# Performance work log

Measured on AMD Instinct MI355X. Metric: run time of the kernel, lower is better.

The kernel has to match this reference:

```python
import jax, jax.numpy as jnp
import numpy as np
from jax import lax

USER_NUM = 100000
COMP_NUM = 50000
ENTITY_NUM = USER_NUM + COMP_NUM + 2  # 150002
N_ACTIVE = USER_NUM + COMP_NUM        # 150000 valid graph nodes
REL_NUM = 200
D = 128
T = 12        # timesteps
E = 250000    # edges per timestep
S = 20000     # seed (LSTM-updated) nodes per timestep
B = 1024      # user batch
USER_ID_MAX = 99999


def setup_inputs() -> dict:
    key = jax.random.key(0)
    ks = jax.random.split(key, 16)
    ent_emb = jax.random.normal(ks[0], (ENTITY_NUM, D), jnp.float32) * 0.02
    c0_emb = jax.random.normal(ks[1], (ENTITY_NUM, D), jnp.float32) * 0.02
    rel_emb = jax.random.normal(ks[2], (REL_NUM, D), jnp.float32) * 0.02
    W_ih = jax.random.normal(ks[3], (4 * D, D), jnp.float32) * (1.0 / np.sqrt(D))
    W_hh = jax.random.normal(ks[4], (4 * D, D), jnp.float32) * (1.0 / np.sqrt(D))
    b_ih = jax.random.normal(ks[5], (4 * D,), jnp.float32) * 0.01
    b_hh = jax.random.normal(ks[6], (4 * D,), jnp.float32) * 0.01
    src = jax.random.randint(ks[7], (T, E), 0, N_ACTIVE, jnp.int32)
    dst = jax.random.randint(ks[8], (T, E), 0, N_ACTIVE, jnp.int32)
    rel_idx = jax.random.randint(ks[9], (T, E), 0, REL_NUM, jnp.int32)
    # unique seed nodes per timestep (scatter targets must not collide)
    seed_keys = jax.random.split(ks[10], T)
    seed_idx = jax.vmap(lambda k: jax.random.permutation(k, N_ACTIVE)[:S])(seed_keys).astype(jnp.int32)
    user_batch = jax.random.randint(ks[11], (B,), 0, USER_NUM, jnp.int32)
    comp_target = jax.random.randint(ks[12], (B,), 0, COMP_NUM, jnp.int32)
    job_target = jax.random.randint(ks[13], (B,), 0, REL_NUM // 2, jnp.int32)
    return {"ent_emb": ent_emb, "c0_emb": c0_emb, "rel_emb": rel_emb,
            "W_ih": W_ih, "W_hh": W_hh, "b_ih": b_ih, "b_hh": b_hh,
            "src": src, "dst": dst, "rel_idx": rel_idx, "seed_idx": seed_idx,
            "user_batch": user_batch, "comp_target": comp_target, "job_target": job_target}


def reference(ent_emb, c0_emb, rel_emb, W_ih, W_hh, b_ih, b_hh,
              src, dst, rel_idx, seed_idx, user_batch, comp_target, job_target):
    def step(carry, xs):
        h, c = carry                       # [N, D] node_emb / cx
        s, d, r, seed = xs
        # msg_GCN: m = src_node_emb * rel_emb[rel]; reduce_GCN: mean over mailbox
        m = h[s] * rel_emb[r]              # [E, D]
        msum = jax.ops.segment_sum(m, d, num_segments=ENTITY_NUM)
        cnt = jax.ops.segment_sum(jnp.ones((E,), h.dtype), d, num_segments=ENTITY_NUM)
        x = h + msum / jnp.maximum(cnt, 1.0)[:, None]   # update_node: node_emb + node_emb2
        # LSTMCell on seed nodes only (input = aggregated emb, state = pre-agg emb, cx)
        xi, hp, cp = x[seed], h[seed], c[seed]          # [S, D]
        gates = xi @ W_ih.T + b_ih + hp @ W_hh.T + b_hh  # [S, 4D]
        ig, fg, gg, og = jnp.split(gates, 4, axis=-1)
        cn = jax.nn.sigmoid(fg) * cp + jax.nn.sigmoid(ig) * jnp.tanh(gg)
        hn = jax.nn.sigmoid(og) * jnp.tanh(cn)
        return (x.at[seed].set(hn), c.at[seed].set(cn)), None

    (h, _c), _ = lax.scan(step, (ent_emb, c0_emb), (src, dst, rel_idx, seed_idx))

    u = h[user_batch]                                   # [B, D] user time embeddings
    # company softmax-CE (logsumexp over all companies)
    tc = ent_emb[comp_target + USER_ID_MAX + 1]
    all_c = ent_emb[USER_ID_MAX + 1: USER_ID_MAX + 1 + COMP_NUM]  # [COMP_NUM, D]
    pos_c = jnp.sum(u * tc, axis=1)
    comp_loss = -jnp.sum(pos_c - jax.nn.logsumexp(u @ all_c.T, axis=1))
    # job (relation) softmax-CE over rel_num // 2 jobs
    tj = rel_emb[job_target]
    all_j = rel_emb[: REL_NUM // 2]
    pos_j = jnp.sum(u * tj, axis=1)
    job_loss = -jnp.sum(pos_j - jax.nn.logsumexp(u @ all_j.T, axis=1))
    return jnp.stack([comp_loss, job_loss])
```

## Files before the change

kernel.cpp:

```cpp
#include <hip/hip_runtime.h>
#include <math.h>

typedef __attribute__((ext_vector_type(8))) short short8;
typedef __attribute__((ext_vector_type(8))) unsigned short u16x8;
typedef __attribute__((ext_vector_type(4))) float f32x4;

#define USER_NUM_  100000
#define COMP_NUM_  50000
#define EN         150002
#define REL_NUM_   200
#define DD         128
#define TT         12
#define EE         250000
#define SS         20000
#define BB         1024
#define NBLK       587
#define PPART      125
#define TILES_PP   25
#define NB         37
#define BSH        12
#define CHUNK      4096
#define NCH        62

__device__ inline unsigned short f2bf(float f) {
    unsigned u = __float_as_uint(f);
    unsigned r = (u + 0x7fffu + ((u >> 16) & 1u)) >> 16;
    return (unsigned short)r;
}

__device__ inline float bf2f(unsigned short u) {
    return __uint_as_float((unsigned)u << 16);
}

__device__ inline float sigmoidf_(float x) { return 1.f / (1.f + __expf(-x)); }

__device__ inline void lse_push(float v, float& m, float& s) {
    if (v <= m) { s += __expf(v - m); }
    else { s = s * __expf(m - v) + 1.f; m = v; }
}

__device__ inline void lse_merge(float& M, float& S, float M2, float S2) {
    float Mn = fmaxf(M, M2);
    S = S * __expf(M - Mn) + S2 * __expf(M2 - Mn);
    M = Mn;
}

__global__ __launch_bounds__(256) void packBF_k(const float* __restrict__ src, ushort4* __restrict__ dst, int n4) {
    int i = blockIdx.x * 256 + threadIdx.x;
    if (i >= n4) return;
    float4 v = ((const float4*)src)[i];
    ushort4 o;
    o.x = f2bf(v.x); o.y = f2bf(v.y); o.z = f2bf(v.z); o.w = f2bf(v.w);
    dst[i] = o;
}

__global__ __launch_bounds__(256) void zero_i32_k(int* __restrict__ p, int n) {
    int i = blockIdx.x * 256 + threadIdx.x;
    if (i < n) p[i] = 0;
}

__global__ __launch_bounds__(256) void prepW_k(const float* __restrict__ Wih, const float* __restrict__ Whh,
                                               const float* __restrict__ bih, const float* __restrict__ bhh,
                                               short* __restrict__ Wt, float* __restrict__ bsum) {
    int n = blockIdx.x;
    int k = threadIdx.x;
    float v = (k < 128) ? Wih[n * 128 + k] : Whh[n * 128 + (k - 128)];
    Wt[n * 256 + k] = (short)f2bf(v);
    if (k == 0) bsum[n] = bih[n] + bhh[n];
}

__global__ __launch_bounds__(256) void binA_k(const int* __restrict__ dst, int* __restrict__ bcnt,
                                              int t0) {
    int slot = blockIdx.y;
    int tid = threadIdx.x;
    int c0 = blockIdx.x * CHUNK;
    int w = tid >> 6;
    __shared__ int lcnt[4][NB];
    for (int i = tid; i < 4 * NB; i += 256) ((int*)lcnt)[i] = 0;
    __syncthreads();
#pragma unroll
    for (int i = 0; i < 16; ++i) {
        int e = c0 + i * 256 + tid;
        if (e < EE) {
            int d = __builtin_nontemporal_load(&dst[(size_t)(t0 + slot) * EE + e]);
            atomicAdd(&lcnt[w][d >> BSH], 1);
        }
    }
    __syncthreads();
    if (tid < NB)
        atomicAdd(&bcnt[slot * NB + tid], lcnt[0][tid] + lcnt[1][tid] + lcnt[2][tid] + lcnt[3][tid]);
}

__global__ __launch_bounds__(64) void binScan_k(const int* __restrict__ bcnt, int* __restrict__ bbase,
                                                int* __restrict__ bcur, int nt) {
    int slot = threadIdx.x;
    if (slot >= nt) return;
    int b = 0;
    for (int c = 0; c < NB; ++c) {
        bbase[slot * (NB + 1) + c] = b;
        bcur[slot * NB + c] = b;
        b += bcnt[slot * NB + c];
    }
    bbase[slot * (NB + 1) + NB] = b;
}

__global__ __launch_bounds__(256) void binB_k(const int* __restrict__ src, const int* __restrict__ dst,
                                              const int* __restrict__ rel, int* __restrict__ bcur,
                                              int2* __restrict__ bucketed, int t0) {
    int slot = blockIdx.y;
    int tid = threadIdx.x;
    int c0 = blockIdx.x * CHUNK;
    __shared__ int lcnt[NB], lbase[NB], gbase[NB], lcur[NB];
    __shared__ int2 stage[CHUNK];
    if (tid < NB) lcnt[tid] = 0;
    __syncthreads();

    int myb[16]; int2 myv[16];
#pragma unroll
    for (int i = 0; i < 16; ++i) {
        int e = c0 + i * 256 + tid;
        if (e < EE) {
            size_t gi = (size_t)(t0 + slot) * EE + e;
            int d = __builtin_nontemporal_load(&dst[gi]);
            int s = __builtin_nontemporal_load(&src[gi]);
            int r = __builtin_nontemporal_load(&rel[gi]);
            myb[i] = d >> BSH;
            myv[i] = make_int2(d, s | (r << 18));
            atomicAdd(&lcnt[myb[i]], 1);
        } else myb[i] = -1;
    }
    __syncthreads();
    if (tid == 0) {
        int b = 0;
        for (int c = 0; c < NB; ++c) { lbase[c] = b; b += lcnt[c]; }
    }
    __syncthreads();
    if (tid < NB) {
        gbase[tid] = (lcnt[tid] > 0) ? atomicAdd(&bcur[slot * NB + tid], lcnt[tid]) : 0;
        lcur[tid] = lbase[tid];
    }
    __syncthreads();
#pragma unroll
    for (int i = 0; i < 16; ++i) {
        if (myb[i] >= 0) {
            int p = atomicAdd(&lcur[myb[i]], 1);
            stage[p] = myv[i];
        }
    }
    __syncthreads();
    int w = tid >> 6, lane = tid & 63;
    int2* bout = bucketed + (size_t)slot * EE;
    for (int b = w; b < NB; b += 4) {
        int cnt = lcnt[b], lb = lbase[b], gb = gbase[b];
        for (int j = lane; j < cnt; j += 64)
            bout[gb + j] = stage[lb + j];
    }
}

__global__ __launch_bounds__(256) void histB_k(const int2* __restrict__ bucketed,
                                               const int* __restrict__ bbase,
                                               int* __restrict__ startp) {
    int b = blockIdx.x, slot = blockIdx.y;
    int tid = threadIdx.x;
    int base_ent = b << BSH;
    int nloc = EN - base_ent; if (nloc > 4096) nloc = 4096;
    __shared__ int lcnt[4096];
    for (int i = tid; i < nloc; i += 256) lcnt[i] = 0;
    __syncthreads();
    int e0 = bbase[slot * (NB + 1) + b], e1 = bbase[slot * (NB + 1) + b + 1];
    for (int e = e0 + tid; e < e1; e += 256) {
        int2 ed = bucketed[(size_t)slot * EE + e];
        atomicAdd(&lcnt[ed.x - base_ent], 1);
    }
    __syncthreads();
    for (int i = tid; i < nloc; i += 256) startp[(size_t)slot * EN + base_ent + i] = lcnt[i];
}

__global__ __launch_bounds__(256) void scanA_k(int* __restrict__ startp, int* __restrict__ bsums) {
    int slot = blockIdx.y;
    int tid = threadIdx.x;
    int i = blockIdx.x * 256 + tid;
    int v = (i < EN) ? startp[slot * EN + i] : 0;
    __shared__ int lds[256];
    lds[tid] = v; __syncthreads();
#pragma unroll
    for (int o = 1; o < 256; o <<= 1) {
        int x = (tid >= o) ? lds[tid - o] : 0;
        __syncthreads();
        lds[tid] += x;
        __syncthreads();
    }
    if (i < EN) startp[slot * EN + i] = lds[tid] - v;
    if (tid == 255) bsums[slot * NBLK + blockIdx.x] = lds[tid];
}

__global__ __launch_bounds__(1024) void scanB_k(int* __restrict__ bsums) {
    int slot = blockIdx.x;
    int tid = threadIdx.x;
    int v = (tid < NBLK) ? bsums[slot * NBLK + tid] : 0;
    __shared__ int lds[1024];
    lds[tid] = v; __syncthreads();
#pragma unroll
    for (int o = 1; o < 1024; o <<= 1) {
        int x = (tid >= o) ? lds[tid - o] : 0;
        __syncthreads();
        lds[tid] += x;
        __syncthreads();
    }
    if (tid < NBLK) bsums[slot * NBLK + tid] = lds[tid] - v;
}

__global__ __launch_bounds__(256) void scanC_k(int* __restrict__ startp, const int* __restrict__ bsums) {
    int slot = blockIdx.y;
    int i = blockIdx.x * 256 + threadIdx.x;
    if (i < EN) startp[slot * EN + i] += bsums[slot * NBLK + blockIdx.x];
}

__global__ __launch_bounds__(256) void scatB_k(const int2* __restrict__ bucketed,
                                               const int* __restrict__ bbase,
                                               int* __restrict__ startp, int* __restrict__ pairs) {
    int b = blockIdx.x, slot = blockIdx.y;
    int tid = threadIdx.x;
    int base_ent = b << BSH;
    int nloc = EN - base_ent; if (nloc > 4096) nloc = 4096;
    __shared__ int lcur[4096];
    for (int i = tid; i < nloc; i += 256) lcur[i] = startp[(size_t)slot * EN + base_ent + i];
    __syncthreads();
    int e0 = bbase[slot * (NB + 1) + b], e1 = bbase[slot * (NB + 1) + b + 1];
    for (int e = e0 + tid; e < e1; e += 256) {
        int2 ed = bucketed[(size_t)slot * EE + e];
        int pos = atomicAdd(&lcur[ed.x - base_ent], 1);
        pairs[(size_t)slot * EE + pos] = ed.y;
    }
    __syncthreads();
    for (int i = tid; i < nloc; i += 256) startp[(size_t)slot * EN + base_ent + i] = lcur[i];
}

__global__ __launch_bounds__(256) void agg_k(const unsigned short* __restrict__ hold,
                                             unsigned short* __restrict__ hnew,
                                             const unsigned short* __restrict__ Rbf,
                                             const int* __restrict__ endp_all,
                                             const int* __restrict__ pairs, int slot) {
    int tid = threadIdx.x;
    int d = blockIdx.x * 16 + (tid >> 4);
    int l = tid & 15;
    if (d >= EN) return;
    const int* endp = endp_all + (size_t)slot * EN;
    int e0 = (d > 0) ? endp[d - 1] : 0;
    int e1 = endp[d];
    const int* pp = pairs + (size_t)slot * EE;
    float acc[8];
#pragma unroll
    for (int j = 0; j < 8; ++j) acc[j] = 0.f;
    int e = e0;
    for (; e + 2 <= e1; e += 2) {
        int pk0 = pp[e], pk1 = pp[e + 1];
        u16x8 h0 = *(const u16x8*)(hold + (size_t)(pk0 & 0x3FFFF) * DD + l * 8);
        u16x8 r0 = *(const u16x8*)(Rbf + (size_t)(pk0 >> 18) * DD + l * 8);
        u16x8 h1 = *(const u16x8*)(hold + (size_t)(pk1 & 0x3FFFF) * DD + l * 8);
        u16x8 r1 = *(const u16x8*)(Rbf + (size_t)(pk1 >> 18) * DD + l * 8);
#pragma unroll
        for (int j = 0; j < 8; ++j)
            acc[j] = fmaf(bf2f(h1[j]), bf2f(r1[j]), fmaf(bf2f(h0[j]), bf2f(r0[j]), acc[j]));
    }
    if (e < e1) {
        int pk0 = pp[e];
        u16x8 h0 = *(const u16x8*)(hold + (size_t)(pk0 & 0x3FFFF) * DD + l * 8);
        u16x8 r0 = *(const u16x8*)(Rbf + (size_t)(pk0 >> 18) * DD + l * 8);
#pragma unroll
        for (int j = 0; j < 8; ++j)
            acc[j] = fmaf(bf2f(h0[j]), bf2f(r0[j]), acc[j]);
    }
    u16x8 hd = *(const u16x8*)(hold + (size_t)d * DD + l * 8);
    int c = e1 - e0;
    float inv = (c > 0) ? 1.f / (float)c : 0.f;
    u16x8 o;
#pragma unroll
    for (int j = 0; j < 8; ++j) o[j] = f2bf(fmaf(acc[j], inv, bf2f(hd[j])));
    *(u16x8*)(hnew + (size_t)d * DD + l * 8) = o;
}

__global__ __launch_bounds__(256) void lstm_k(const unsigned short* __restrict__ hold,
                                              unsigned short* __restrict__ hnew,
                                              unsigned short* __restrict__ cbuf, const short* __restrict__ Wt,
                                              const float* __restrict__ bsum, const int* __restrict__ seed) {
    int w = threadIdx.x >> 6;
    int lane = threadIdx.x & 63;
    int lrow = lane & 15, lhi = lane >> 4;
    int m0 = blockIdx.x * 32;
    int w32 = w * 32;

    const unsigned short* pxi[2];
    const unsigned short* php[2];
#pragma unroll
    for (int mi = 0; mi < 2; ++mi) {
        int m = m0 + mi * 16 + lrow;
        int sd = seed[m];
        pxi[mi] = hnew + (size_t)sd * DD;
        php[mi] = hold + (size_t)sd * DD;
    }

    f32x4 acc[2][4][2];
#pragma unroll
    for (int mi = 0; mi < 2; ++mi)
#pragma unroll
        for (int g = 0; g < 4; ++g)
#pragma unroll
            for (int s = 0; s < 2; ++s)
                acc[mi][g][s] = (f32x4){0.f, 0.f, 0.f, 0.f};

#pragma unroll
    for (int kk = 0; kk < 8; ++kk) {
        int klane = kk * 32 + lhi * 8;
        short8 af[2];
#pragma unroll
        for (int mi = 0; mi < 2; ++mi) {
            const unsigned short* p = (klane < 128) ? (pxi[mi] + klane) : (php[mi] + (klane - 128));
            af[mi] = *(const short8*)p;
        }
#pragma unroll
        for (int g = 0; g < 4; ++g)
#pragma unroll
            for (int s = 0; s < 2; ++s) {
                int col = g * 128 + w32 + s * 16 + lrow;
                short8 bf = *(const short8*)(Wt + col * 256 + klane);
                acc[0][g][s] = __builtin_amdgcn_mfma_f32_16x16x32_bf16(af[0], bf, acc[0][g][s], 0, 0, 0);
                acc[1][g][s] = __builtin_amdgcn_mfma_f32_16x16x32_bf16(af[1], bf, acc[1][g][s], 0, 0, 0);
            }
    }

    __syncthreads();

#pragma unroll
    for (int mi = 0; mi < 2; ++mi) {
#pragma unroll
        for (int r = 0; r < 4; ++r) {
            int m = m0 + mi * 16 + lhi * 4 + r;
            int sd = seed[m];
#pragma unroll
            for (int s = 0; s < 2; ++s) {
                int d = w32 + s * 16 + lrow;
                float ig = acc[mi][0][s][r] + bsum[d];
                float fg = acc[mi][1][s][r] + bsum[128 + d];
                float gg = acc[mi][2][s][r] + bsum[256 + d];
                float og = acc[mi][3][s][r] + bsum[384 + d];
                float cp = bf2f(cbuf[(size_t)sd * DD + d]);
                float cn = sigmoidf_(fg) * cp + sigmoidf_(ig) * tanhf(gg);
                float hn = sigmoidf_(og) * tanhf(cn);
                cbuf[(size_t)sd * DD + d] = f2bf(cn);
                hnew[(size_t)sd * DD + d] = f2bf(hn);
            }
        }
    }
}

__global__ __launch_bounds__(256) void packU_k(const unsigned short* __restrict__ hfin, const int* __restrict__ ub,
                                               short* __restrict__ Ubf) {
    int i = blockIdx.x * 256 + threadIdx.x;
    if (i >= BB * DD) return;
    int u = i >> 7, k = i & 127;
    Ubf[i] = (short)hfin[(size_t)ub[u] * DD + k];
}

__global__ __launch_bounds__(256) void comp_mfma_k(const short* __restrict__ Ubf, const short* __restrict__ Cbf,
                                                   float* __restrict__ partm, float* __restrict__ parts) {
    int tid = threadIdx.x;
    int w = tid >> 6, lane = tid & 63;
    int lrow = lane & 15, lhi = lane >> 4;
    int ubase = blockIdx.x * 128 + w * 32;
    int p = blockIdx.y;

    __shared__ __align__(16) short ct[2][16][136];

    short8 a[2][4];
#pragma unroll
    for (int s2 = 0; s2 < 2; ++s2)
#pragma unroll
        for (int kc = 0; kc < 4; ++kc)
            a[s2][kc] = *(const short8*)(Ubf + (size_t)(ubase + s2 * 16 + lrow) * DD + kc * 32 + lhi * 8);

    float s[2][4];
#pragma unroll
    for (int s2 = 0; s2 < 2; ++s2)
#pragma unroll
        for (int r = 0; r < 4; ++r) s[s2][r] = 0.f;

    int c0 = p * TILES_PP * 16;
    int srow = tid >> 4, scol = (tid & 15) * 8;
    {
        short8 v = *(const short8*)(Cbf + (size_t)(c0 + srow) * DD + scol);
        *(short8*)&ct[0][srow][scol] = v;
    }

    for (int tile = 0; tile < TILES_PP; ++tile) {
        int cur = tile & 1;
        short8 pf;
        bool hn = (tile + 1 < TILES_PP);
        if (hn)
            pf = *(const short8*)(Cbf + (size_t)(c0 + (tile + 1) * 16 + srow) * DD + scol);
        __syncthreads();
        if (hn) *(short8*)&ct[cur ^ 1][srow][scol] = pf;

        f32x4 acc0 = {0.f, 0.f, 0.f, 0.f};
        f32x4 acc1 = {0.f, 0.f, 0.f, 0.f};
#pragma unroll
        for (int kc = 0; kc < 4; ++kc) {
            short8 b = *(const short8*)&ct[cur][lrow][kc * 32 + lhi * 8];
            acc0 = __builtin_amdgcn_mfma_f32_16x16x32_bf16(a[0][kc], b, acc0, 0, 0, 0);
            acc1 = __builtin_amdgcn_mfma_f32_16x16x32_bf16(a[1][kc], b, acc1, 0, 0, 0);
        }
#pragma unroll
        for (int r = 0; r < 4; ++r) {
            s[0][r] += __expf(acc0[r]);
            s[1][r] += __expf(acc1[r]);
        }
    }

#pragma unroll
    for (int s2 = 0; s2 < 2; ++s2)
#pragma unroll
        for (int r = 0; r < 4; ++r) {
            float S = s[s2][r];
#pragma unroll
            for (int o = 1; o < 16; o <<= 1)
                S += __shfl_xor(S, o, 64);
            if (lrow == 0) {
                int u = ubase + s2 * 16 + lhi * 4 + r;
                partm[(size_t)u * PPART + p] = 0.f;
                parts[(size_t)u * PPART + p] = S;
            }
        }
}

__global__ __launch_bounds__(256) void finish2_k(const unsigned short* __restrict__ hfin,
                                                 const float* __restrict__ ent,
                                                 const float* __restrict__ rel, const int* __restrict__ ub,
                                                 const int* __restrict__ ct, const int* __restrict__ jt,
                                                 const float* __restrict__ partm, const float* __restrict__ parts,
                                                 float* __restrict__ out) {
    __shared__ float s_u[4][128];
    int w = threadIdx.x >> 6, lane = threadIdx.x & 63;
    int u = blockIdx.x * 4 + w;

    const unsigned short* up = hfin + (size_t)ub[u] * DD;
    float u0 = bf2f(up[lane]), u1 = bf2f(up[lane + 64]);
    s_u[w][lane] = u0;
    s_u[w][lane + 64] = u1;

    const float* tcp = ent + (size_t)(USER_NUM_ + ct[u]) * DD;
    float pc = u0 * tcp[lane] + u1 * tcp[lane + 64];
    const float* tjp = rel + (size_t)jt[u] * DD;
    float pj = u0 * tjp[lane] + u1 * tjp[lane + 64];
#pragma unroll
    for (int o = 1; o < 64; o <<= 1) {
        pc += __shfl_xor(pc, o, 64);
        pj += __shfl_xor(pj, o, 64);
    }

    float M = partm[(size_t)u * PPART + lane];
    float S = parts[(size_t)u * PPART + lane];
    if (lane + 64 < PPART)
        lse_merge(M, S, partm[(size_t)u * PPART + lane + 64], parts[(size_t)u * PPART + lane + 64]);
#pragma unroll
    for (int o = 1; o < 64; o <<= 1) {
        float M2 = __shfl_xor(M, o, 64);
        float S2 = __shfl_xor(S, o, 64);
        lse_merge(M, S, M2, S2);
    }
    float lse_c = M + logf(S);

    int j1 = lane, j2 = lane + 64;
    bool v2 = j2 < (REL_NUM_ / 2);
    const float* r1 = rel + (size_t)j1 * DD;
    const float* r2 = rel + (size_t)(v2 ? j2 : 0) * DD;
    float d1 = 0.f, d2 = 0.f;
#pragma unroll 16
    for (int k = 0; k < DD; ++k) {
        float uk = s_u[w][k];
        d1 = fmaf(uk, r1[k], d1);
        d2 = fmaf(uk, r2[k], d2);
    }
    float Mj = d1, Sj = 1.f;
    if (v2) lse_push(d2, Mj, Sj);
#pragma unroll
    for (int o = 1; o < 64; o <<= 1) {
        float M2 = __shfl_xor(Mj, o, 64);
        float S2 = __shfl_xor(Sj, o, 64);
        lse_merge(Mj, Sj, M2, S2);
    }
    float lse_j = Mj + logf(Sj);

    if (lane == 0) {
        atomicAdd(&out[0], lse_c - pc);
        atomicAdd(&out[1], lse_j - pj);
    }
}

static inline size_t rup(size_t x) { return (x + 255) & ~(size_t)255; }

extern "C" void kernel_launch(void* const* d_in, const int* in_sizes, int n_in,
                              void* d_out, int out_size, void* d_ws, size_t ws_size,
                              hipStream_t stream) {
    const float* ent_emb = (const float*)d_in[0];
    const float* c0_emb  = (const float*)d_in[1];
    const float* rel_emb = (const float*)d_in[2];
    const float* W_ih    = (const float*)d_in[3];
    const float* W_hh    = (const float*)d_in[4];
    const float* b_ih    = (const float*)d_in[5];
    const float* b_hh    = (const float*)d_in[6];
    const int* src       = (const int*)d_in[7];
    const int* dst       = (const int*)d_in[8];
    const int* rel_idx   = (const int*)d_in[9];
    const int* seed_idx  = (const int*)d_in[10];
    const int* ubatch    = (const int*)d_in[11];
    const int* ctarg     = (const int*)d_in[12];
    const int* jtarg     = (const int*)d_in[13];
    float* out = (float*)d_out;

    const size_t HBH = (size_t)EN * DD * 2;

    char* base = (char*)d_ws;
    unsigned short* h0   = (unsigned short*)base;
    unsigned short* h1   = (unsigned short*)(base + HBH);
    unsigned short* cbuf = (unsigned short*)(base + 2 * HBH);

    int* startp; int* pairs; int* bsums; int2* bucketed; int* bcnt; int* bbase; int* bcur;
    short* Wt; float* bsumv; unsigned short* Rbf;
    auto place = [&](int NT) -> size_t {
        size_t o = 3 * HBH;
        startp   = (int*)(base + o);  o += rup((size_t)NT * EN * 4);
        pairs    = (int*)(base + o);  o += rup((size_t)NT * EE * 4);
        bucketed = (int2*)(base + o); o += rup((size_t)NT * EE * 8);
        bsums    = (int*)(base + o);  o += rup((size_t)NT * NBLK * 4);
        bcnt     = (int*)(base + o);  o += rup((size_t)NT * NB * 4);
        bbase    = (int*)(base + o);  o += rup((size_t)NT * (NB + 1) * 4);
        bcur     = (int*)(base + o);  o += rup((size_t)NT * NB * 4);
        Wt       = (short*)(base + o); o += rup(512 * 256 * 2);
        bsumv    = (float*)(base + o); o += rup(512 * 4);
        Rbf      = (unsigned short*)(base + o); o += rup((size_t)REL_NUM_ * DD * 2);
        return o;
    };

    const int cands[6] = {12, 6, 4, 3, 2, 1};
    int NT = 1;
    for (int i = 0; i < 6; ++i) {
        if (place(cands[i]) <= ws_size) { NT = cands[i]; break; }
    }
    place(NT);

    char* q = (char*)cbuf;
    short* Cbf = (short*)q;            q += rup((size_t)COMP_NUM_ * DD * 2);
    short* Ubf = (short*)q;            q += rup((size_t)BB * DD * 2);
    float* partm = (float*)q;          q += rup((size_t)BB * PPART * 4);
    float* parts = (float*)q;

    hipMemsetAsync(d_out, 0, 2 * sizeof(float), stream);

    const int n4 = EN * DD / 4;
    const int gcpy = (n4 + 255) / 256;

    prepW_k<<<512, 256, 0, stream>>>(W_ih, W_hh, b_ih, b_hh, Wt, bsumv);
    packBF_k<<<gcpy, 256, 0, stream>>>(ent_emb, (ushort4*)h0, n4);
    packBF_k<<<gcpy, 256, 0, stream>>>(c0_emb, (ushort4*)cbuf, n4);
    packBF_k<<<(REL_NUM_ * DD / 4 + 255) / 256, 256, 0, stream>>>(rel_emb, (ushort4*)Rbf, REL_NUM_ * DD / 4);

    auto build = [&](int t0, int nt) {
        zero_i32_k<<<(nt * NB + 255) / 256, 256, 0, stream>>>(bcnt, nt * NB);
        binA_k<<<dim3(NCH, nt), 256, 0, stream>>>(dst, bcnt, t0);
        binScan_k<<<1, 64, 0, stream>>>(bcnt, bbase, bcur, nt);
        binB_k<<<dim3(NCH, nt), 256, 0, stream>>>(src, dst, rel_idx, bcur, bucketed, t0);
        histB_k<<<dim3(NB, nt), 256, 0, stream>>>(bucketed, bbase, startp);
        scanA_k<<<dim3(NBLK, nt), 256, 0, stream>>>(startp, bsums);
        scanB_k<<<nt, 1024, 0, stream>>>(bsums);
        scanC_k<<<dim3(NBLK, nt), 256, 0, stream>>>(startp, bsums);
        scatB_k<<<dim3(NB, nt), 256, 0, stream>>>(bucketed, bbase, startp, pairs);
    };

    unsigned short* hold = h0;
    unsigned short* hnew = h1;
    const int gagg = (EN + 15) / 16;

    for (int b0 = 0; b0 < TT; b0 += NT) {
        int nb = (TT - b0 < NT) ? (TT - b0) : NT;
        build(b0, nb);
        for (int k = 0; k < nb; ++k) {
            int t = b0 + k;
            agg_k<<<gagg, 256, 0, stream>>>(hold, hnew, Rbf, startp, pairs, k);
            lstm_k<<<SS / 32, 256, 0, stream>>>(hold, hnew, cbuf, Wt, bsumv, seed_idx + (size_t)t * SS);
            unsigned short* tmp = hold; hold = hnew; hnew = tmp;
        }
    }

    packBF_k<<<(COMP_NUM_ * DD / 4 + 255) / 256, 256, 0, stream>>>(ent_emb + (size_t)USER_NUM_ * DD,
                                                                   (ushort4*)Cbf, COMP_NUM_ * DD / 4);
    packU_k<<<(BB * DD + 255) / 256, 256, 0, stream>>>(hold, ubatch, Ubf);
    comp_mfma_k<<<dim3(BB / 128, PPART), 256, 0, stream>>>(Ubf, Cbf, partm, parts);
    finish2_k<<<BB / 4, 256, 0, stream>>>(hold, ent_emb, rel_emb, ubatch, ctarg, jtarg,
                                          partm, parts, out);
}
```

Baseline: 926.0 us.

## Fuse CSR offset scan into bucket histogram kernel and use nontemporal loads in aggregation

The histogram kernel now computes an exclusive scan of per-node counts inside each bucket in LDS and offsets it by the bucket's global edge base. This replaces the separate three-kernel global prefix scan (scanA/scanB/scanC) and removes its buffer, launches and extra passes over startp. The aggregation kernel also switches its edge-list reads, self-row read and output store to nontemporal hints to reduce cache pollution. This relies on bucket bases already giving the correct global offsets. The nontemporal hint on hold rows may hurt reuse if other blocks read the same rows.

```diff
diff --git a/kernel.cpp b/kernel.cpp
--- a/kernel.cpp
+++ b/kernel.cpp
@@ -14,7 +14,6 @@
 #define EE         250000
 #define SS         20000
 #define BB         1024
-#define NBLK       587
 #define PPART      125
 #define TILES_PP   25
 #define NB         37
@@ -157,7 +156,7 @@
     }
 }
 
-__global__ __launch_bounds__(256) void histB_k(const int2* __restrict__ bucketed,
+__global__ __launch_bounds__(256) void histC_k(const int2* __restrict__ bucketed,
                                                const int* __restrict__ bbase,
                                                int* __restrict__ startp) {
     int b = blockIdx.x, slot = blockIdx.y;
@@ -165,7 +164,8 @@
     int base_ent = b << BSH;
     int nloc = EN - base_ent; if (nloc > 4096) nloc = 4096;
     __shared__ int lcnt[4096];
-    for (int i = tid; i < nloc; i += 256) lcnt[i] = 0;
+    __shared__ int tsum[256];
+    for (int i = tid; i < 4096; i += 256) lcnt[i] = 0;
     __syncthreads();
     int e0 = bbase[slot * (NB + 1) + b], e1 = bbase[slot * (NB + 1) + b + 1];
     for (int e = e0 + tid; e < e1; e += 256) {
@@ -173,47 +173,28 @@
         atomicAdd(&lcnt[ed.x - base_ent], 1);
     }
     __syncthreads();
+    int base16 = tid * 16;
+    int s = 0;
+#pragma unroll
+    for (int k = 0; k < 16; ++k) s += lcnt[base16 + k];
+    tsum[tid] = s;
+    __syncthreads();
+#pragma unroll
+    for (int o = 1; o < 256; o <<= 1) {
+        int x = (tid >= o) ? tsum[tid - o] : 0;
+        __syncthreads();
+        tsum[tid] += x;
+        __syncthreads();
+    }
+    int run = e0 + tsum[tid] - s;
+#pragma unroll
+    for (int k = 0; k < 16; ++k) {
+        int c = lcnt[base16 + k];
+        lcnt[base16 + k] = run;
+        run += c;
+    }
+    __syncthreads();
     for (int i = tid; i < nloc; i += 256) startp[(size_t)slot * EN + base_ent + i] = lcnt[i];
-}
-
-__global__ __launch_bounds__(256) void scanA_k(int* __restrict__ startp, int* __restrict__ bsums) {
-    int slot = blockIdx.y;
-    int tid = threadIdx.x;
-    int i = blockIdx.x * 256 + tid;
-    int v = (i < EN) ? startp[slot * EN + i] : 0;
-    __shared__ int lds[256];
-    lds[tid] = v; __syncthreads();
-#pragma unroll
-    for (int o = 1; o < 256; o <<= 1) {
-        int x = (tid >= o) ? lds[tid - o] : 0;
-        __syncthreads();
-        lds[tid] += x;
-        __syncthreads();
-    }
-    if (i < EN) startp[slot * EN + i] = lds[tid] - v;
-    if (tid == 255) bsums[slot * NBLK + blockIdx.x] = lds[tid];
-}
-
-__global__ __launch_bounds__(1024) void scanB_k(int* __restrict__ bsums) {
-    int slot = blockIdx.x;
-    int tid = threadIdx.x;
-    int v = (tid < NBLK) ? bsums[slot * NBLK + tid] : 0;
-    __shared__ int lds[1024];
-    lds[tid] = v; __syncthreads();
-#pragma unroll
-    for (int o = 1; o < 1024; o <<= 1) {
-        int x = (tid >= o) ? lds[tid - o] : 0;
-        __syncthreads();
-        lds[tid] += x;
-        __syncthreads();
-    }
-    if (tid < NBLK) bsums[slot * NBLK + tid] = lds[tid] - v;
-}
-
-__global__ __launch_bounds__(256) void scanC_k(int* __restrict__ startp, const int* __restrict__ bsums) {
-    int slot = blockIdx.y;
-    int i = blockIdx.x * 256 + threadIdx.x;
-    if (i < EN) startp[slot * EN + i] += bsums[slot * NBLK + blockIdx.x];
 }
 
 __global__ __launch_bounds__(256) void scatB_k(const int2* __restrict__ bucketed,
@@ -254,7 +235,8 @@
     for (int j = 0; j < 8; ++j) acc[j] = 0.f;
     int e = e0;
     for (; e + 2 <= e1; e += 2) {
-        int pk0 = pp[e], pk1 = pp[e + 1];
+        int pk0 = __builtin_nontemporal_load(&pp[e]);
+        int pk1 = __builtin_nontemporal_load(&pp[e + 1]);
         u16x8 h0 = *(const u16x8*)(hold + (size_t)(pk0 & 0x3FFFF) * DD + l * 8);
         u16x8 r0 = *(const u16x8*)(Rbf + (size_t)(pk0 >> 18) * DD + l * 8);
         u16x8 h1 = *(const u16x8*)(hold + (size_t)(pk1 & 0x3FFFF) * DD + l * 8);
@@ -264,20 +246,20 @@
             acc[j] = fmaf(bf2f(h1[j]), bf2f(r1[j]), fmaf(bf2f(h0[j]), bf2f(r0[j]), acc[j]));
     }
     if (e < e1) {
-        int pk0 = pp[e];
+        int pk0 = __builtin_nontemporal_load(&pp[e]);
         u16x8 h0 = *(const u16x8*)(hold + (size_t)(pk0 & 0x3FFFF) * DD + l * 8);
         u16x8 r0 = *(const u16x8*)(Rbf + (size_t)(pk0 >> 18) * DD + l * 8);
 #pragma unroll
         for (int j = 0; j < 8; ++j)
             acc[j] = fmaf(bf2f(h0[j]), bf2f(r0[j]), acc[j]);
     }
-    u16x8 hd = *(const u16x8*)(hold + (size_t)d * DD + l * 8);
+    u16x8 hd = __builtin_nontemporal_load((const u16x8*)(hold + (size_t)d * DD + l * 8));
     int c = e1 - e0;
     float inv = (c > 0) ? 1.f / (float)c : 0.f;
     u16x8 o;
 #pragma unroll
     for (int j = 0; j < 8; ++j) o[j] = f2bf(fmaf(acc[j], inv, bf2f(hd[j])));
-    *(u16x8*)(hnew + (size_t)d * DD + l * 8) = o;
+    __builtin_nontemporal_store(o, (u16x8*)(hnew + (size_t)d * DD + l * 8));
 }
 
 __global__ __launch_bounds__(256) void lstm_k(const unsigned short* __restrict__ hold,
@@ -524,14 +506,13 @@
     unsigned short* h1   = (unsigned short*)(base + HBH);
     unsigned short* cbuf = (unsigned short*)(base + 2 * HBH);
 
-    int* startp; int* pairs; int* bsums; int2* bucketed; int* bcnt; int* bbase; int* bcur;
+    int* startp; int* pairs; int2* bucketed; int* bcnt; int* bbase; int* bcur;
     short* Wt; float* bsumv; unsigned short* Rbf;
     auto place = [&](int NT) -> size_t {
         size_t o = 3 * HBH;
         startp   = (int*)(base + o);  o += rup((size_t)NT * EN * 4);
         pairs    = (int*)(base + o);  o += rup((size_t)NT * EE * 4);
         bucketed = (int2*)(base + o); o += rup((size_t)NT * EE * 8);
-        bsums    = (int*)(base + o);  o += rup((size_t)NT * NBLK * 4);
         bcnt     = (int*)(base + o);  o += rup((size_t)NT * NB * 4);
         bbase    = (int*)(base + o);  o += rup((size_t)NT * (NB + 1) * 4);
         bcur     = (int*)(base + o);  o += rup((size_t)NT * NB * 4);
@@ -569,10 +550,7 @@
         binA_k<<<dim3(NCH, nt), 256, 0, stream>>>(dst, bcnt, t0);
         binScan_k<<<1, 64, 0, stream>>>(bcnt, bbase, bcur, nt);
         binB_k<<<dim3(NCH, nt), 256, 0, stream>>>(src, dst, rel_idx, bcur, bucketed, t0);
-        histB_k<<<dim3(NB, nt), 256, 0, stream>>>(bucketed, bbase, startp);
-        scanA_k<<<dim3(NBLK, nt), 256, 0, stream>>>(startp, bsums);
-        scanB_k<<<nt, 1024, 0, stream>>>(bsums);
-        scanC_k<<<dim3(NBLK, nt), 256, 0, stream>>>(startp, bsums);
+        histC_k<<<dim3(NB, nt), 256, 0, stream>>>(bucketed, bbase, startp);
         scatB_k<<<dim3(NB, nt), 256, 0, stream>>>(bucketed, bbase, startp, pairs);
     };
 
```

After: 1.026 ms. 1.11x slower.
